# Kernel optimization log

Hardware: AMD Instinct MI355X
Metric: run time of the kernel (lower is better)

The kernel has to match this reference:

```python
import jax, jax.numpy as jnp
import numpy as np
from jax.ops import segment_sum, segment_max

N = 100000      # nodes
E = 1600000     # directed edges (before self loops)
H = 4           # attention heads
DIMS = [128, 128, 128, 64]
NEG_SLOPE = 0.2


def setup_inputs() -> dict:
    key = jax.random.key(0)
    ks = jax.random.split(key, 20)
    inp = {}
    inp['x'] = jax.random.normal(ks[0], (N, DIMS[0]), jnp.float32)
    inp['edge_index'] = jax.random.randint(ks[1], (2, E), 0, N, jnp.int32)
    k = 2
    for i in range(3):
        ind, outd = DIMS[i], DIMS[i + 1]
        hd = outd // H
        s = 1.0 / np.sqrt(ind)
        inp[f'W{i}'] = jax.random.uniform(ks[k], (ind, outd), jnp.float32, -s, s); k += 1
        inp[f'a_src{i}'] = jax.random.uniform(ks[k], (H, hd), jnp.float32, -s, s); k += 1
        inp[f'a_dst{i}'] = jax.random.uniform(ks[k], (H, hd), jnp.float32, -s, s); k += 1
        inp[f'b{i}'] = jnp.zeros((outd,), jnp.float32)
    s = 1.0 / np.sqrt(DIMS[-1])
    inp['Wc'] = jax.random.uniform(ks[k], (DIMS[-1], 40), jnp.float32, -s, s)
    inp['bc'] = jnp.zeros((40,), jnp.float32)
    return inp


def _gat_layer(x, W, a_src, a_dst, b, src, dst):
    n = x.shape[0]
    hd = a_src.shape[1]
    h = (x @ W).reshape(n, H, hd)                       # [N,H,hd]
    # per-node attention logits (computed once, gathered per edge)
    al_s = (h * a_src[None]).sum(-1)                    # [N,H]
    al_d = (h * a_dst[None]).sum(-1)                    # [N,H]
    e = jax.nn.leaky_relu(al_s[src] + al_d[dst], NEG_SLOPE)   # [E,H]
    # segment softmax over incoming edges of each destination node
    m = segment_max(e, dst, num_segments=n)             # [N,H]
    ex = jnp.exp(e - m[dst])                            # [E,H]
    denom = segment_sum(ex, dst, num_segments=n)        # [N,H]
    alpha = ex / (denom[dst] + 1e-16)                   # [E,H]
    msg = alpha[:, :, None] * h[src]                    # [E,H,hd]
    out = segment_sum(msg, dst, num_segments=n)         # [N,H,hd]
    return out.reshape(n, H * hd) + b


def reference(x, W0, a_src0, a_dst0, b0, W1, a_src1, a_dst1, b1,
              W2, a_src2, a_dst2, b2, Wc, bc, edge_index):
    n = x.shape[0]
    loops = jnp.arange(n, dtype=edge_index.dtype)       # PyG add_self_loops=True
    src = jnp.concatenate([edge_index[0], loops])
    dst = jnp.concatenate([edge_index[1], loops])
    params = [(W0, a_src0, a_dst0, b0), (W1, a_src1, a_dst1, b1), (W2, a_src2, a_dst2, b2)]
    h = x
    for (W, a_s, a_d, b) in params:
        h = jax.nn.relu(_gat_layer(h, W, a_s, a_d, b, src, dst))
    return h @ Wc + bc
```

## Files before the change

### kernel.cpp

```cpp
#include <hip/hip_runtime.h>
#include <hip/hip_bf16.h>
#include <hip/hip_fp16.h>
#include <stdint.h>

typedef __hip_bfloat16 bf16;
typedef _Float16 f16;
typedef __attribute__((ext_vector_type(8))) _Float16 f16x8;
typedef __attribute__((ext_vector_type(4))) _Float16 f16x4;
typedef __attribute__((ext_vector_type(2))) _Float16 f16x2;
typedef __attribute__((ext_vector_type(4))) float    f32x4;

__device__ __forceinline__ float us2f(uint16_t u){
  union { uint32_t i; float f; } v; v.i = ((uint32_t)u) << 16; return v.f;
}
__device__ __forceinline__ float bflo(uint32_t u){
  union { uint32_t i; float f; } v; v.i = u << 16; return v.f;
}
__device__ __forceinline__ float bfhi(uint32_t u){
  union { uint32_t i; float f; } v; v.i = u & 0xffff0000u; return v.f;
}
__device__ __forceinline__ uint16_t f2u16(float f){
  union { bf16 b; uint16_t u; } v; v.b = __float2bfloat16(f); return v.u;
}
struct h16 { uint16_t v; };

__device__ __forceinline__ float  ldh (const float* p, size_t i){ return p[i]; }
__device__ __forceinline__ float  ldh (const uint16_t* p, size_t i){ return us2f(p[i]); }
__device__ __forceinline__ float  ldh (const h16* p, size_t i){ return __half2float(((const __half*)p)[i]); }
__device__ __forceinline__ float2 ldh2(const float* p, size_t i){ return ((const float2*)p)[i]; }
__device__ __forceinline__ float2 ldh2(const uint16_t* p, size_t i){
  uint32_t u = ((const uint32_t*)p)[i]; return make_float2(bflo(u), bfhi(u));
}
__device__ __forceinline__ float2 ldh2(const h16* p, size_t i){
  __half2 u = ((const __half2*)p)[i];
  return make_float2(__low2float(u), __high2float(u));
}
__device__ __forceinline__ void sth (float* p, size_t i, float v){ p[i] = v; }
__device__ __forceinline__ void sth (uint16_t* p, size_t i, float v){ p[i] = f2u16(v); }
__device__ __forceinline__ void sth (h16* p, size_t i, float v){ ((__half*)p)[i] = __float2half(v); }
__device__ __forceinline__ void sth2(float* p, size_t i, float2 v){ ((float2*)p)[i] = v; }
__device__ __forceinline__ void sth2(uint16_t* p, size_t i, float2 v){
  ((uint32_t*)p)[i] = (uint32_t)f2u16(v.x) | ((uint32_t)f2u16(v.y) << 16);
}
__device__ __forceinline__ void sth2(h16* p, size_t i, float2 v){
  ((__half2*)p)[i] = __float22half2_rn(v);
}
template<typename T> struct vtt { using t = float; };
template<> struct vtt<h16> { using t = f16; };

__device__ __forceinline__ void ld4(const float* p, size_t i4, float* o){
  float4 v = ((const float4*)p)[i4]; o[0]=v.x; o[1]=v.y; o[2]=v.z; o[3]=v.w;
}
__device__ __forceinline__ void ld4(const uint16_t* p, size_t i4, float* o){
  uint2 u = ((const uint2*)p)[i4];
  o[0]=bflo(u.x); o[1]=bfhi(u.x); o[2]=bflo(u.y); o[3]=bfhi(u.y);
}
__device__ __forceinline__ void ld4(const h16* p, size_t i4, f16* o){
  f16x4 v = ((const f16x4*)p)[i4];
  o[0]=v[0]; o[1]=v[1]; o[2]=v[2]; o[3]=v[3];
}
__device__ __forceinline__ void ld2v(const float* p, size_t i2, float* o){
  float2 v = ((const float2*)p)[i2]; o[0]=v.x; o[1]=v.y;
}
__device__ __forceinline__ void ld2v(const uint16_t* p, size_t i2, float* o){
  uint32_t u = ((const uint32_t*)p)[i2]; o[0]=bflo(u); o[1]=bfhi(u);
}
__device__ __forceinline__ void ld2v(const h16* p, size_t i2, f16* o){
  f16x2 v = ((const f16x2*)p)[i2]; o[0]=v[0]; o[1]=v[1];
}
__device__ __forceinline__ void st4(float* p, size_t i4, const float* o){
  ((float4*)p)[i4] = make_float4(o[0],o[1],o[2],o[3]);
}
__device__ __forceinline__ void st4(uint16_t* p, size_t i4, const float* o){
  uint2 u;
  u.x = (uint32_t)f2u16(o[0]) | ((uint32_t)f2u16(o[1]) << 16);
  u.y = (uint32_t)f2u16(o[2]) | ((uint32_t)f2u16(o[3]) << 16);
  ((uint2*)p)[i4] = u;
}
__device__ __forceinline__ void st4(h16* p, size_t i4, const float* o){
  ((__half2*)p)[i4*2]   = __float22half2_rn(make_float2(o[0],o[1]));
  ((__half2*)p)[i4*2+1] = __float22half2_rn(make_float2(o[2],o[3]));
}
__device__ __forceinline__ void ld8(const float* p, size_t i, float* o){
  float4 a = ((const float4*)(p+i))[0];
  float4 b = ((const float4*)(p+i))[1];
  o[0]=a.x; o[1]=a.y; o[2]=a.z; o[3]=a.w; o[4]=b.x; o[5]=b.y; o[6]=b.z; o[7]=b.w;
}
__device__ __forceinline__ void ld8(const uint16_t* p, size_t i, float* o){
  uint4 u = *(const uint4*)(p+i);
  o[0]=bflo(u.x); o[1]=bfhi(u.x); o[2]=bflo(u.y); o[3]=bfhi(u.y);
  o[4]=bflo(u.z); o[5]=bfhi(u.z); o[6]=bflo(u.w); o[7]=bfhi(u.w);
}
__device__ __forceinline__ void ld8(const h16* p, size_t i, float* o){
  const __half2* q = (const __half2*)(p+i);
  #pragma unroll
  for (int j=0;j<4;j++){ __half2 u=q[j]; o[2*j]=__low2float(u); o[2*j+1]=__high2float(u); }
}

__global__ void detect2_kernel(const uint32_t* __restrict__ x, const uint32_t* __restrict__ ei,
                               int* __restrict__ flag, int* __restrict__ eflag){
  int t = threadIdx.x;
  if (t < 64){
    uint32_t w = x[t];
    uint32_t e = (w >> 7) & 0xffu;
    bool looks_bf16 = (e >= 118 && e <= 134);
    unsigned long long m = __ballot(looks_bf16);
    if (t == 0) flag[0] = (__popcll(m) >= 32) ? 0 : 1;
  } else {
    int lane = t - 64;
    uint32_t w = ei[lane];
    bool ok = (lane & 1) ? (w == 0u) : true;
    unsigned long long m = __ballot(ok);
    if (lane == 0) eflag[0] = (__popcll(m) == 64) ? 1 : 0;
  }
}

struct PP {
  const void* src[14];
  int off[14];
  int cnt[14];
};

__global__ void cvt_params_kernel(PP pp, float* __restrict__ dst, const int* __restrict__ flag){
  int b = blockIdx.x;
  int cnt = pp.cnt[b];
  float* d = dst + pp.off[b];
  if (flag[0] != 0){
    const float* s = (const float*)pp.src[b];
    for (int i = threadIdx.x; i < cnt; i += 256) d[i] = s[i];
  } else {
    const uint16_t* s = (const uint16_t*)pp.src[b];
    for (int i = threadIdx.x; i < cnt; i += 256) d[i] = us2f(s[i]);
  }
}

struct WF {
  int src[4];
  int dst[4];
  int cnt[4];
  int K[4], Ms[4], Mp[4];
  int blk0[5];
};

__global__ void wfrag4_kernel(const float* __restrict__ prm, uint16_t* __restrict__ whl, WF wf){
  int b = blockIdx.x;
  int w = 3;
  if (b < wf.blk0[1]) w = 0; else if (b < wf.blk0[2]) w = 1; else if (b < wf.blk0[3]) w = 2;
  int e = (b - wf.blk0[w])*256 + threadIdx.x;
  int CT = wf.Mp[w] >> 4, KC = wf.K[w] >> 5;
  if (e >= KC*CT*64) return;
  const float* W = prm + wf.src[w];
  uint16_t* wh = whl + wf.dst[w];
  uint16_t* wl = wh + wf.cnt[w];
  int Ms = wf.Ms[w];
  int l = e & 63, t = e >> 6;
  int ct = t % CT, c = t / CT;
  int kbase = c*32 + (l>>4)*8;
  int m = ct*16 + (l&15);
  #pragma unroll
  for (int i=0;i<8;i++){
    float v = (m < Ms) ? W[(size_t)(kbase+i)*Ms + m] : 0.f;
    f16 h = (f16)v;
    f16 r = (f16)(v - (float)h);
    union { f16 f; uint16_t u; } ch, cr; ch.f = h; cr.f = r;
    wh[(size_t)e*8 + i] = ch.u;
    wl[(size_t)e*8 + i] = cr.u;
  }
}

__global__ void count_kernel(const int* __restrict__ ei, const int* __restrict__ eflag,
                             int* __restrict__ counts, int* __restrict__ rank,
                             int E, int n){
  int i = blockIdx.x * 256 + threadIdx.x;
  if (i >= E + n) return;
  int d;
  if (i < E) d = eflag[0] ? ei[2*(size_t)E + 2*(size_t)i] : ei[(size_t)E + i];
  else       d = i - E;
  rank[i] = atomicAdd(&counts[d], 1);
}

#define SCAN_BS 256
#define SCAN_CHUNK 1024

__global__ void scan1_kernel(const int* __restrict__ counts, int* __restrict__ offs,
                             int* __restrict__ bsums, int n){
  __shared__ int sdata[SCAN_BS];
  int b = blockIdx.x, t = threadIdx.x;
  int base = b * SCAN_CHUNK + t * 4;
  int v[4]; int s = 0;
  #pragma unroll
  for (int j=0;j<4;j++){ int idx = base+j; v[j] = (idx<n)? counts[idx] : 0; s += v[j]; }
  sdata[t] = s;
  __syncthreads();
  for (int off=1; off<SCAN_BS; off<<=1){
    int x = (t>=off)? sdata[t-off] : 0;
    __syncthreads();
    sdata[t] += x;
    __syncthreads();
  }
  int run = sdata[t] - s;
  #pragma unroll
  for (int j=0;j<4;j++){ int idx = base+j; if (idx<n) offs[idx] = run; run += v[j]; }
  if (t == SCAN_BS-1) bsums[b] = sdata[t];
}

__global__ void scan2_kernel(int* __restrict__ bsums, int nb){
  __shared__ int sdata[1024];
  int t = threadIdx.x;
  int v = (t<nb)? bsums[t] : 0;
  sdata[t] = v;
  __syncthreads();
  for (int off=1; off<1024; off<<=1){
    int x = (t>=off)? sdata[t-off] : 0;
    __syncthreads();
    sdata[t] += x;
    __syncthreads();
  }
  if (t<nb) bsums[t] = sdata[t] - v;
}

__global__ void scan3_kernel(int* __restrict__ offs, const int* __restrict__ bsums,
                             int n, int total){
  int i = blockIdx.x * 256 + threadIdx.x;
  if (i < n) offs[i] += bsums[i / SCAN_CHUNK];
  if (i == n) offs[n] = total;
}

__global__ void fill_kernel(const int* __restrict__ ei, const int* __restrict__ eflag,
                            const int* __restrict__ offs, const int* __restrict__ rank,
                            int* __restrict__ csr, int E, int n){
  int i = blockIdx.x * 256 + threadIdx.x;
  if (i >= E + n) return;
  int s, d;
  if (i < E){
    if (eflag[0]){ s = ei[2*(size_t)i]; d = ei[2*(size_t)E + 2*(size_t)i]; }
    else         { s = ei[i];           d = ei[(size_t)E + i]; }
  } else { s = i - E; d = i - E; }
  csr[offs[d] + rank[i]] = s;
}

template<int K, int M, bool DET, typename TA, typename TC>
__global__ __launch_bounds__(256) void gemm_mfma(const void* __restrict__ Ap,
    const uint16_t* __restrict__ whb, const uint16_t* __restrict__ wlb,
    TC* __restrict__ C, int n, const int* __restrict__ flag){
  constexpr int CT = M/16;
  constexpr int KC = K/32;
  constexpr int RT = 2;
  int tid = threadIdx.x;
  int wv  = tid >> 6, l = tid & 63;
  int lr  = l & 15, kg = l >> 4;
  int r0  = blockIdx.x*(64*RT) + wv*(16*RT);

  bool f32 = DET ? (flag[0] != 0) : false;
  const uint16_t* Au = (const uint16_t*)Ap;
  const float*    Af = (const float*)Ap;
  const TA*       At = (const TA*)Ap;
  const f16x8* Wh = (const f16x8*)whb;
  const f16x8* Wl = (const f16x8*)wlb;

  f32x4 acc[RT][CT];
  #pragma unroll
  for (int rt=0;rt<RT;rt++)
    #pragma unroll
    for (int ct=0;ct<CT;ct++) acc[rt][ct] = (f32x4){0.f,0.f,0.f,0.f};

  for (int c=0; c<KC; c++){
    f16x8 ah[RT], al[RT];
    #pragma unroll
    for (int rt=0;rt<RT;rt++){
      int arow = r0 + rt*16 + lr;
      if (arow > n-1) arow = n-1;
      size_t idx = (size_t)arow*K + c*32 + kg*8;
      float av[8];
      if (DET){
        if (f32) ld8(Af, idx, av);
        else     ld8(Au, idx, av);
      } else {
        ld8(At, idx, av);
      }
      #pragma unroll
      for (int i=0;i<8;i++){
        f16 h = (f16)av[i];
        ah[rt][i] = h;
        al[rt][i] = (f16)(av[i] - (float)h);
      }
    }
    #pragma unroll
    for (int ct=0;ct<CT;ct++){
      f16x8 bh = Wh[(size_t)(c*CT + ct)*64 + l];
      f16x8 bl = Wl[(size_t)(c*CT + ct)*64 + l];
      #pragma unroll
      for (int rt=0;rt<RT;rt++){
        acc[rt][ct] = __builtin_amdgcn_mfma_f32_16x16x32_f16(ah[rt], bh, acc[rt][ct], 0, 0, 0);
        acc[rt][ct] = __builtin_amdgcn_mfma_f32_16x16x32_f16(al[rt], bh, acc[rt][ct], 0, 0, 0);
        acc[rt][ct] = __builtin_amdgcn_mfma_f32_16x16x32_f16(ah[rt], bl, acc[rt][ct], 0, 0, 0);
      }
    }
  }

  #pragma unroll
  for (int rt=0;rt<RT;rt++){
    #pragma unroll
    for (int r=0;r<4;r++){
      int orow = r0 + rt*16 + kg*4 + r;
      if (orow < n){
        #pragma unroll
        for (int ct=0;ct<CT;ct++)
          sth(C, (size_t)orow*M + ct*16 + lr, acc[rt][ct][r]);
      }
    }
  }
}

template<typename TA>
__global__ __launch_bounds__(256) void gemm_cls(const TA* __restrict__ A,
    const uint16_t* __restrict__ whb, const uint16_t* __restrict__ wlb,
    const float* __restrict__ bc, float* __restrict__ out, int n){
  constexpr int CT = 3, KC = 2, RT = 2;
  int tid = threadIdx.x;
  int wv  = tid >> 6, l = tid & 63;
  int lr  = l & 15, kg = l >> 4;
  int r0  = blockIdx.x*128 + wv*32;
  const f16x8* Wh = (const f16x8*)whb;
  const f16x8* Wl = (const f16x8*)wlb;

  f32x4 acc[RT][CT];
  #pragma unroll
  for (int rt=0;rt<RT;rt++)
    #pragma unroll
    for (int ct=0;ct<CT;ct++) acc[rt][ct] = (f32x4){0.f,0.f,0.f,0.f};

  for (int c=0; c<KC; c++){
    f16x8 ah[RT], al[RT];
    #pragma unroll
    for (int rt=0;rt<RT;rt++){
      int arow = r0 + rt*16 + lr;
      if (arow > n-1) arow = n-1;
      size_t idx = (size_t)arow*64 + c*32 + kg*8;
      float av[8];
      ld8(A, idx, av);
      #pragma unroll
      for (int i=0;i<8;i++){
        f16 h = (f16)av[i];
        ah[rt][i] = h;
        al[rt][i] = (f16)(av[i] - (float)h);
      }
    }
    #pragma unroll
    for (int ct=0;ct<CT;ct++){
      f16x8 bh = Wh[(size_t)(c*CT + ct)*64 + l];
      f16x8 bl = Wl[(size_t)(c*CT + ct)*64 + l];
      #pragma unroll
      for (int rt=0;rt<RT;rt++){
        acc[rt][ct] = __builtin_amdgcn_mfma_f32_16x16x32_f16(ah[rt], bh, acc[rt][ct], 0, 0, 0);
        acc[rt][ct] = __builtin_amdgcn_mfma_f32_16x16x32_f16(al[rt], bh, acc[rt][ct], 0, 0, 0);
        acc[rt][ct] = __builtin_amdgcn_mfma_f32_16x16x32_f16(ah[rt], bl, acc[rt][ct], 0, 0, 0);
      }
    }
  }

  #pragma unroll
  for (int rt=0;rt<RT;rt++){
    #pragma unroll
    for (int r=0;r<4;r++){
      int orow = r0 + rt*16 + kg*4 + r;
      if (orow < n){
        #pragma unroll
        for (int ct=0;ct<CT;ct++){
          int col = ct*16 + lr;
          if (col < 40)
            out[(size_t)orow*40 + col] = acc[rt][ct][r] + bc[col];
        }
      }
    }
  }
}

template<int OUTD, int HD, typename T>
__global__ void logits_kernel(const T* __restrict__ hW, const float* __restrict__ a_src,
                              const float* __restrict__ a_dst, float* __restrict__ als,
                              float* __restrict__ ald, int n){
  int i = blockIdx.x * 256 + threadIdx.x;
  if (i >= n*4) return;
  int node = i >> 2, h = i & 3;
  const T* hp = hW + (size_t)node*OUTD + h*HD;
  float ss = 0.f, sd = 0.f;
  #pragma unroll
  for (int d2=0; d2<HD/2; d2++){
    float2 v = ldh2(hp, d2);
    int b = h*HD + 2*d2;
    ss += v.x*a_src[b] + v.y*a_src[b+1];
    sd += v.x*a_dst[b] + v.y*a_dst[b+1];
  }
  als[i] = ss; ald[i] = sd;
}

template<int OUTD, typename TIN, typename TOUT>
__global__ __launch_bounds__(256) void aggregate_kernel(const TIN* __restrict__ hW,
            const float* __restrict__ als, const float* __restrict__ ald,
            const int* __restrict__ offs, const int* __restrict__ csr,
            const float* __restrict__ bias, TOUT* __restrict__ hout, int n){
  constexpr int VEC = OUTD / 32;
  using VT = typename vtt<TIN>::t;
  int wid = (blockIdx.x * 256 + threadIdx.x) >> 6;
  if (wid >= n) return;
  int lane = threadIdx.x & 63;
  int half = lane >> 5;
  int l2   = lane & 31;
  int h    = l2 >> 3;
  int beg = offs[wid], end = offs[wid+1];
  float adh = ald[(size_t)wid*4 + h];

  float acc[VEC];
  #pragma unroll
  for (int k=0;k<VEC;k++) acc[k] = 0.f;
  float den = 0.f;

  int last = end - 1;
  for (int j = beg + half; j < end; j += 8){
    int j1 = j+2, j2 = j+4, j3 = j+6;
    bool p1 = j1 < end, p2 = j2 < end, p3 = j3 < end;
    int s0 = csr[j];
    int s1 = csr[p1 ? j1 : last];
    int s2 = csr[p2 ? j2 : last];
    int s3 = csr[p3 ? j3 : last];
    VT v0[VEC], v1[VEC], v2[VEC], v3[VEC];
    if constexpr (VEC == 4){
      ld4(hW, (size_t)s0*32 + l2, v0);
      ld4(hW, (size_t)s1*32 + l2, v1);
      ld4(hW, (size_t)s2*32 + l2, v2);
      ld4(hW, (size_t)s3*32 + l2, v3);
    } else {
      ld2v(hW, (size_t)s0*32 + l2, v0);
      ld2v(hW, (size_t)s1*32 + l2, v1);
      ld2v(hW, (size_t)s2*32 + l2, v2);
      ld2v(hW, (size_t)s3*32 + l2, v3);
    }
    float e0 = als[(size_t)s0*4 + h] + adh;
    float e1 = als[(size_t)s1*4 + h] + adh;
    float e2 = als[(size_t)s2*4 + h] + adh;
    float e3 = als[(size_t)s3*4 + h] + adh;
    e0 = (e0>0.f)? e0 : 0.2f*e0;
    e1 = (e1>0.f)? e1 : 0.2f*e1;
    e2 = (e2>0.f)? e2 : 0.2f*e2;
    e3 = (e3>0.f)? e3 : 0.2f*e3;
    float ex0 = __expf(e0);
    float ex1 = p1 ? __expf(e1) : 0.f;
    float ex2 = p2 ? __expf(e2) : 0.f;
    float ex3 = p3 ? __expf(e3) : 0.f;
    den += (ex0 + ex1) + (ex2 + ex3);
    #pragma unroll
    for (int k=0;k<VEC;k++){
      acc[k] = fmaf(ex0, (float)v0[k], acc[k]);
      acc[k] = fmaf(ex1, (float)v1[k], acc[k]);
      acc[k] = fmaf(ex2, (float)v2[k], acc[k]);
      acc[k] = fmaf(ex3, (float)v3[k], acc[k]);
    }
  }

  den += __shfl_xor(den, 32);
  #pragma unroll
  for (int k=0;k<VEC;k++) acc[k] += __shfl_xor(acc[k], 32);

  if (half == 0){
    float inv = 1.f / (den + 1e-16f);
    float o[VEC];
    if constexpr (VEC == 4){
      const float4 bv = ((const float4*)bias)[l2];
      o[0] = fmaf(acc[0], inv, bv.x);
      o[1] = fmaf(acc[1], inv, bv.y);
      o[2] = fmaf(acc[2], inv, bv.z);
      o[3] = fmaf(acc[3], inv, bv.w);
      #pragma unroll
      for (int k=0;k<4;k++) o[k] = (o[k]>0.f)? o[k] : 0.f;
      st4(hout, (size_t)wid*32 + l2, o);
    } else {
      const float2 bv = ((const float2*)bias)[l2];
      o[0] = fmaf(acc[0], inv, bv.x);
      o[1] = fmaf(acc[1], inv, bv.y);
      o[0] = (o[0]>0.f)? o[0] : 0.f;
      o[1] = (o[1]>0.f)? o[1] : 0.f;
      sth2(hout, (size_t)wid*32 + l2, make_float2(o[0], o[1]));
    }
  }
}

template<typename TM, typename TO>
static void run_pipeline(void* const* d_in, int ei_idx, int pbase, int n, int E,
                         void* d_out, int out_size, void* d_ws, size_t ws_size,
                         hipStream_t stream){
  const void* x = d_in[0];
  const int* ei = (const int*)d_in[ei_idx];
  float* out = (float*)d_out;
  int Etot = E + n;

  char* p = (char*)d_ws;
  auto alloc = [&](size_t bytes)->char* {
    char* r = p; p += (bytes + 255) & ~(size_t)255; return r;
  };
  int*   flag   = (int*)  alloc(256);
  int*   eflag  = (int*)  alloc(256);
  int*   counts = (int*)  alloc((size_t)n * 4);
  float* als    = (float*)alloc((size_t)n * 16);
  float* ald    = (float*)alloc((size_t)n * 16);
  float* prm    = (float*)alloc(48000 * 4);
  uint16_t* whl = (uint16_t*)alloc(88064 * 2);

  size_t csr_b  = ((size_t)Etot * 4 + 255) & ~(size_t)255;
  size_t offs_b = ((size_t)(n + 1) * 4 + 255) & ~(size_t)255;
  size_t rank_b = ((size_t)Etot * 4 + 255) & ~(size_t)255;
  size_t out_bytes = (size_t)out_size * 4;
  int *csr, *offs, *rank, *bsums;
  if (csr_b + offs_b + rank_b + 4096 <= out_bytes){
    char* q = (char*)d_out;
    csr   = (int*)q;
    offs  = (int*)(q + csr_b);
    rank  = (int*)(q + csr_b + offs_b);
    bsums = (int*)(q + csr_b + offs_b + rank_b);
  } else {
    csr   = (int*)alloc((size_t)Etot * 4);
    offs  = (int*)alloc((size_t)(n + 1) * 4);
    rank  = (int*)alloc((size_t)Etot * 4);
    bsums = (int*)alloc(4096);
  }
  TM* bufMid = (TM*)alloc((size_t)n * 128 * sizeof(TM));
  TO* bufOut = (TO*)alloc((size_t)n * 128 * sizeof(TO));

  PP pp;
  static const int cnts[14] = {16384,128,128,128, 16384,128,128,128, 8192,64,64,64, 2560,40};
  int off = 0;
  for (int i = 0; i < 14; i++){
    pp.src[i] = d_in[pbase + i];
    pp.cnt[i] = cnts[i];
    pp.off[i] = off;
    off += cnts[i];
  }
  const float* W0  = prm + pp.off[0];
  const float* as0 = prm + pp.off[1];
  const float* ad0 = prm + pp.off[2];
  const float* b0  = prm + pp.off[3];
  const float* as1 = prm + pp.off[5];
  const float* ad1 = prm + pp.off[6];
  const float* b1  = prm + pp.off[7];
  const float* as2 = prm + pp.off[9];
  const float* ad2 = prm + pp.off[10];
  const float* b2  = prm + pp.off[11];
  const float* bc  = prm + pp.off[13];

  uint16_t* wh0 = whl;
  uint16_t* wl0 = whl + 16384;
  uint16_t* wh1 = whl + 32768;
  uint16_t* wl1 = whl + 49152;
  uint16_t* wh2 = whl + 65536;
  uint16_t* wl2 = whl + 73728;
  uint16_t* whc = whl + 81920;
  uint16_t* wlc = whl + 84992;

  hipMemsetAsync(counts, 0, (size_t)n * 4, stream);

  detect2_kernel<<<1, 128, 0, stream>>>((const uint32_t*)x, (const uint32_t*)ei, flag, eflag);
  cvt_params_kernel<<<14, 256, 0, stream>>>(pp, prm, flag);

  WF wf;
  wf.src[0]=pp.off[0]; wf.src[1]=pp.off[4]; wf.src[2]=pp.off[8]; wf.src[3]=pp.off[12];
  wf.dst[0]=0; wf.dst[1]=32768; wf.dst[2]=65536; wf.dst[3]=81920;
  wf.cnt[0]=16384; wf.cnt[1]=16384; wf.cnt[2]=8192; wf.cnt[3]=3072;
  wf.K[0]=128; wf.K[1]=128; wf.K[2]=128; wf.K[3]=64;
  wf.Ms[0]=128; wf.Ms[1]=128; wf.Ms[2]=64; wf.Ms[3]=40;
  wf.Mp[0]=128; wf.Mp[1]=128; wf.Mp[2]=64; wf.Mp[3]=48;
  wf.blk0[0]=0; wf.blk0[1]=8; wf.blk0[2]=16; wf.blk0[3]=20; wf.blk0[4]=22;
  wfrag4_kernel<<<22, 256, 0, stream>>>(prm, whl, wf);

  count_kernel<<<(Etot + 255)/256, 256, 0, stream>>>(ei, eflag, counts, rank, E, n);
  int nb = (n + SCAN_CHUNK - 1) / SCAN_CHUNK;
  scan1_kernel<<<nb, SCAN_BS, 0, stream>>>(counts, offs, bsums, n);
  scan2_kernel<<<1, 1024, 0, stream>>>(bsums, nb);
  scan3_kernel<<<(n + 1 + 255)/256, 256, 0, stream>>>(offs, bsums, n, Etot);
  fill_kernel<<<(Etot + 255)/256, 256, 0, stream>>>(ei, eflag, offs, rank, csr, E, n);

  int gg   = (n + 127) / 128;
  int log_grid = (n*4 + 255) / 256;
  int agg_grid = (n + 3) / 4;

  gemm_mfma<128,128,true,TO,TM><<<gg, 256, 0, stream>>>(x, wh0, wl0, bufMid, n, flag);
  logits_kernel<128,32,TM><<<log_grid, 256, 0, stream>>>(bufMid, as0, ad0, als, ald, n);
  aggregate_kernel<128,TM,TO><<<agg_grid, 256, 0, stream>>>(bufMid, als, ald, offs, csr, b0, bufOut, n);

  gemm_mfma<128,128,false,TO,TM><<<gg, 256, 0, stream>>>(bufOut, wh1, wl1, bufMid, n, flag);
  logits_kernel<128,32,TM><<<log_grid, 256, 0, stream>>>(bufMid, as1, ad1, als, ald, n);
  aggregate_kernel<128,TM,TO><<<agg_grid, 256, 0, stream>>>(bufMid, als, ald, offs, csr, b1, bufOut, n);

  gemm_mfma<128,64,false,TO,TM><<<gg, 256, 0, stream>>>(bufOut, wh2, wl2, bufMid, n, flag);
  logits_kernel<64,16,TM><<<log_grid, 256, 0, stream>>>(bufMid, as2, ad2, als, ald, n);
  aggregate_kernel<64,TM,TO><<<agg_grid, 256, 0, stream>>>(bufMid, als, ald, offs, csr, b2, bufOut, n);

  gemm_cls<TO><<<gg, 256, 0, stream>>>(bufOut, whc, wlc, bc, out, n);
}

extern "C" void kernel_launch(void* const* d_in, const int* in_sizes, int n_in,
                              void* d_out, int out_size, void* d_ws, size_t ws_size,
                              hipStream_t stream) {
  int n = in_sizes[0] / 128;

  int ei_idx, pbase;
  if (n_in >= 2 && in_sizes[1] > 1000000) { ei_idx = 1;        pbase = 2; }
  else                                    { ei_idx = n_in - 1; pbase = 1; }
  int E = in_sizes[ei_idx] / 2;

  size_t base = 512
              + (((size_t)n*4  + 255) & ~(size_t)255)
              + 2*(((size_t)n*16 + 255) & ~(size_t)255)
              + ((48000*4 + 255) & ~(size_t)255)
              + ((88064*2 + 255) & ~(size_t)255)
              + 65536
              + 3*(((size_t)(E + n)*4 + 255) & ~(size_t)255);
  size_t f32buf  = ((size_t)n*128*4 + 255) & ~(size_t)255;
  size_t h16buf  = ((size_t)n*128*2 + 255) & ~(size_t)255;

  if (ws_size >= base + f32buf + h16buf)
    run_pipeline<h16, float>(d_in, ei_idx, pbase, n, E, d_out, out_size, d_ws, ws_size, stream);
  else
    run_pipeline<h16, uint16_t>(d_in, ei_idx, pbase, n, E, d_out, out_size, d_ws, ws_size, stream);
}
```

Before: 555.9 us.

## Fold attention logits into GEMM via extra W·a columns

Precomputes W·a_src and W·a_dst per head as eight extra weight columns, padded to a 16-wide MFMA tile, so each layer's GEMM emits the per-node source and destination logits directly. This removes the three separate logits kernels and their re-read of the projected features. The cost is one more column tile of MFMA work per GEMM and a larger weight-fragment buffer. Logits are now computed from the fp32 GEMM accumulation instead of from the stored half-precision features, which changes rounding slightly.

```diff
diff --git a/kernel.cpp b/kernel.cpp
--- a/kernel.cpp
+++ b/kernel.cpp
@@ -139,6 +139,7 @@
   int dst[4];
   int cnt[4];
   int K[4], Ms[4], Mp[4];
+  int as_off[4], ad_off[4], hd[4];
   int blk0[5];
 };
 
@@ -159,7 +160,21 @@
   int m = ct*16 + (l&15);
   #pragma unroll
   for (int i=0;i<8;i++){
-    float v = (m < Ms) ? W[(size_t)(kbase+i)*Ms + m] : 0.f;
+    int k = kbase + i;
+    float v = 0.f;
+    if (m < Ms){
+      v = W[(size_t)k*Ms + m];
+    } else {
+      int j = m - Ms;
+      if (wf.as_off[w] >= 0 && j < 8){
+        const float* a = prm + ((j < 4) ? wf.as_off[w] : wf.ad_off[w]);
+        int head = j & 3, hd = wf.hd[w];
+        float s = 0.f;
+        for (int tt=0; tt<hd; tt++)
+          s = fmaf(W[(size_t)k*Ms + head*hd + tt], a[head*hd + tt], s);
+        v = s;
+      }
+    }
     f16 h = (f16)v;
     f16 r = (f16)(v - (float)h);
     union { f16 f; uint16_t u; } ch, cr; ch.f = h; cr.f = r;
@@ -242,10 +257,12 @@
 template<int K, int M, bool DET, typename TA, typename TC>
 __global__ __launch_bounds__(256) void gemm_mfma(const void* __restrict__ Ap,
     const uint16_t* __restrict__ whb, const uint16_t* __restrict__ wlb,
-    TC* __restrict__ C, int n, const int* __restrict__ flag){
-  constexpr int CT = M/16;
-  constexpr int KC = K/32;
-  constexpr int RT = 2;
+    TC* __restrict__ C, float* __restrict__ als, float* __restrict__ ald,
+    int n, const int* __restrict__ flag){
+  constexpr int CT  = M/16;
+  constexpr int CTX = CT + 1;
+  constexpr int KC  = K/32;
+  constexpr int RT  = 2;
   int tid = threadIdx.x;
   int wv  = tid >> 6, l = tid & 63;
   int lr  = l & 15, kg = l >> 4;
@@ -258,11 +275,11 @@
   const f16x8* Wh = (const f16x8*)whb;
   const f16x8* Wl = (const f16x8*)wlb;
 
-  f32x4 acc[RT][CT];
+  f32x4 acc[RT][CTX];
   #pragma unroll
   for (int rt=0;rt<RT;rt++)
     #pragma unroll
-    for (int ct=0;ct<CT;ct++) acc[rt][ct] = (f32x4){0.f,0.f,0.f,0.f};
+    for (int ct=0;ct<CTX;ct++) acc[rt][ct] = (f32x4){0.f,0.f,0.f,0.f};
 
   for (int c=0; c<KC; c++){
     f16x8 ah[RT], al[RT];
@@ -286,9 +303,9 @@
       }
     }
     #pragma unroll
-    for (int ct=0;ct<CT;ct++){
-      f16x8 bh = Wh[(size_t)(c*CT + ct)*64 + l];
-      f16x8 bl = Wl[(size_t)(c*CT + ct)*64 + l];
+    for (int ct=0;ct<CTX;ct++){
+      f16x8 bh = Wh[(size_t)(c*CTX + ct)*64 + l];
+      f16x8 bl = Wl[(size_t)(c*CTX + ct)*64 + l];
       #pragma unroll
       for (int rt=0;rt<RT;rt++){
         acc[rt][ct] = __builtin_amdgcn_mfma_f32_16x16x32_f16(ah[rt], bh, acc[rt][ct], 0, 0, 0);
@@ -307,6 +324,9 @@
         #pragma unroll
         for (int ct=0;ct<CT;ct++)
           sth(C, (size_t)orow*M + ct*16 + lr, acc[rt][ct][r]);
+        float ev = acc[rt][CT][r];
+        if (lr < 4)      als[(size_t)orow*4 + lr]     = ev;
+        else if (lr < 8) ald[(size_t)orow*4 + lr - 4] = ev;
       }
     }
   }
@@ -374,25 +394,6 @@
       }
     }
   }
-}
-
-template<int OUTD, int HD, typename T>
-__global__ void logits_kernel(const T* __restrict__ hW, const float* __restrict__ a_src,
-                              const float* __restrict__ a_dst, float* __restrict__ als,
-                              float* __restrict__ ald, int n){
-  int i = blockIdx.x * 256 + threadIdx.x;
-  if (i >= n*4) return;
-  int node = i >> 2, h = i & 3;
-  const T* hp = hW + (size_t)node*OUTD + h*HD;
-  float ss = 0.f, sd = 0.f;
-  #pragma unroll
-  for (int d2=0; d2<HD/2; d2++){
-    float2 v = ldh2(hp, d2);
-    int b = h*HD + 2*d2;
-    ss += v.x*a_src[b] + v.y*a_src[b+1];
-    sd += v.x*a_dst[b] + v.y*a_dst[b+1];
-  }
-  als[i] = ss; ald[i] = sd;
 }
 
 template<int OUTD, typename TIN, typename TOUT>
@@ -504,7 +505,7 @@
   float* als    = (float*)alloc((size_t)n * 16);
   float* ald    = (float*)alloc((size_t)n * 16);
   float* prm    = (float*)alloc(48000 * 4);
-  uint16_t* whl = (uint16_t*)alloc(88064 * 2);
+  uint16_t* whl = (uint16_t*)alloc(100352 * 2);
 
   size_t csr_b  = ((size_t)Etot * 4 + 255) & ~(size_t)255;
   size_t offs_b = ((size_t)(n + 1) * 4 + 255) & ~(size_t)255;
@@ -535,26 +536,19 @@
     pp.off[i] = off;
     off += cnts[i];
   }
-  const float* W0  = prm + pp.off[0];
-  const float* as0 = prm + pp.off[1];
-  const float* ad0 = prm + pp.off[2];
   const float* b0  = prm + pp.off[3];
-  const float* as1 = prm + pp.off[5];
-  const float* ad1 = prm + pp.off[6];
   const float* b1  = prm + pp.off[7];
-  const float* as2 = prm + pp.off[9];
-  const float* ad2 = prm + pp.off[10];
   const float* b2  = prm + pp.off[11];
   const float* bc  = prm + pp.off[13];
 
   uint16_t* wh0 = whl;
-  uint16_t* wl0 = whl + 16384;
-  uint16_t* wh1 = whl + 32768;
-  uint16_t* wl1 = whl + 49152;
-  uint16_t* wh2 = whl + 65536;
-  uint16_t* wl2 = whl + 73728;
-  uint16_t* whc = whl + 81920;
-  uint16_t* wlc = whl + 84992;
+  uint16_t* wl0 = whl + 18432;
+  uint16_t* wh1 = whl + 36864;
+  uint16_t* wl1 = whl + 55296;
+  uint16_t* wh2 = whl + 73728;
+  uint16_t* wl2 = whl + 83968;
+  uint16_t* whc = whl + 94208;
+  uint16_t* wlc = whl + 97280;
 
   hipMemsetAsync(counts, 0, (size_t)n * 4, stream);
 
@@ -563,13 +557,16 @@
 
   WF wf;
   wf.src[0]=pp.off[0]; wf.src[1]=pp.off[4]; wf.src[2]=pp.off[8]; wf.src[3]=pp.off[12];
-  wf.dst[0]=0; wf.dst[1]=32768; wf.dst[2]=65536; wf.dst[3]=81920;
-  wf.cnt[0]=16384; wf.cnt[1]=16384; wf.cnt[2]=8192; wf.cnt[3]=3072;
+  wf.dst[0]=0; wf.dst[1]=36864; wf.dst[2]=73728; wf.dst[3]=94208;
+  wf.cnt[0]=18432; wf.cnt[1]=18432; wf.cnt[2]=10240; wf.cnt[3]=3072;
   wf.K[0]=128; wf.K[1]=128; wf.K[2]=128; wf.K[3]=64;
   wf.Ms[0]=128; wf.Ms[1]=128; wf.Ms[2]=64; wf.Ms[3]=40;
-  wf.Mp[0]=128; wf.Mp[1]=128; wf.Mp[2]=64; wf.Mp[3]=48;
-  wf.blk0[0]=0; wf.blk0[1]=8; wf.blk0[2]=16; wf.blk0[3]=20; wf.blk0[4]=22;
-  wfrag4_kernel<<<22, 256, 0, stream>>>(prm, whl, wf);
+  wf.Mp[0]=144; wf.Mp[1]=144; wf.Mp[2]=80; wf.Mp[3]=48;
+  wf.as_off[0]=pp.off[1]; wf.as_off[1]=pp.off[5]; wf.as_off[2]=pp.off[9];  wf.as_off[3]=-1;
+  wf.ad_off[0]=pp.off[2]; wf.ad_off[1]=pp.off[6]; wf.ad_off[2]=pp.off[10]; wf.ad_off[3]=-1;
+  wf.hd[0]=32; wf.hd[1]=32; wf.hd[2]=16; wf.hd[3]=0;
+  wf.blk0[0]=0; wf.blk0[1]=9; wf.blk0[2]=18; wf.blk0[3]=23; wf.blk0[4]=25;
+  wfrag4_kernel<<<25, 256, 0, stream>>>(prm, whl, wf);
 
   count_kernel<<<(Etot + 255)/256, 256, 0, stream>>>(ei, eflag, counts, rank, E, n);
   int nb = (n + SCAN_CHUNK - 1) / SCAN_CHUNK;
@@ -579,19 +576,15 @@
   fill_kernel<<<(Etot + 255)/256, 256, 0, stream>>>(ei, eflag, offs, rank, csr, E, n);
 
   int gg   = (n + 127) / 128;
-  int log_grid = (n*4 + 255) / 256;
   int agg_grid = (n + 3) / 4;
 
-  gemm_mfma<128,128,true,TO,TM><<<gg, 256, 0, stream>>>(x, wh0, wl0, bufMid, n, flag);
-  logits_kernel<128,32,TM><<<log_grid, 256, 0, stream>>>(bufMid, as0, ad0, als, ald, n);
+  gemm_mfma<128,128,true,TO,TM><<<gg, 256, 0, stream>>>(x, wh0, wl0, bufMid, als, ald, n, flag);
   aggregate_kernel<128,TM,TO><<<agg_grid, 256, 0, stream>>>(bufMid, als, ald, offs, csr, b0, bufOut, n);
 
-  gemm_mfma<128,128,false,TO,TM><<<gg, 256, 0, stream>>>(bufOut, wh1, wl1, bufMid, n, flag);
-  logits_kernel<128,32,TM><<<log_grid, 256, 0, stream>>>(bufMid, as1, ad1, als, ald, n);
+  gemm_mfma<128,128,false,TO,TM><<<gg, 256, 0, stream>>>(bufOut, wh1, wl1, bufMid, als, ald, n, flag);
   aggregate_kernel<128,TM,TO><<<agg_grid, 256, 0, stream>>>(bufMid, als, ald, offs, csr, b1, bufOut, n);
 
-  gemm_mfma<128,64,false,TO,TM><<<gg, 256, 0, stream>>>(bufOut, wh2, wl2, bufMid, n, flag);
-  logits_kernel<64,16,TM><<<log_grid, 256, 0, stream>>>(bufMid, as2, ad2, als, ald, n);
+  gemm_mfma<128,64,false,TO,TM><<<gg, 256, 0, stream>>>(bufOut, wh2, wl2, bufMid, als, ald, n, flag);
   aggregate_kernel<64,TM,TO><<<agg_grid, 256, 0, stream>>>(bufMid, als, ald, offs, csr, b2, bufOut, n);
 
   gemm_cls<TO><<<gg, 256, 0, stream>>>(bufOut, whc, wlc, bc, out, n);
@@ -611,7 +604,7 @@
               + (((size_t)n*4  + 255) & ~(size_t)255)
               + 2*(((size_t)n*16 + 255) & ~(size_t)255)
               + ((48000*4 + 255) & ~(size_t)255)
-              + ((88064*2 + 255) & ~(size_t)255)
+              + ((100352*2 + 255) & ~(size_t)255)
               + 65536
               + 3*(((size_t)(E + n)*4 + 255) & ~(size_t)255);
   size_t f32buf  = ((size_t)n*128*4 + 255) & ~(size_t)255;
```

Measured after the change: 542.6 us. 2.4% less time.
